# Kernel optimization log

Measured on AMD Instinct MI355X. Metric: run time of the kernel, lower is better.

The kernel has to match this reference:

```python
import jax, jax.numpy as jnp
import numpy as np
import math

LOG2 = math.log(2.0)

def shifted_softplus(x):
    return jax.nn.softplus(x) - LOG2

def setup_inputs() -> dict:
    key = jax.random.key(0)
    ks = jax.random.split(key, 12)
    n_atoms, n_pairs = 40000, 640000
    d_basis, d_filt, n_rbf = 128, 128, 20
    x = jax.random.normal(ks[0], (n_atoms, d_basis), dtype=jnp.float32)
    f_ij = jax.random.uniform(ks[1], (n_pairs, n_rbf), dtype=jnp.float32)
    idx_i = jax.random.randint(ks[2], (n_pairs,), 0, n_atoms)
    idx_j = jax.random.randint(ks[3], (n_pairs,), 0, n_atoms)
    rcut_ij = jax.random.uniform(ks[4], (n_pairs,), dtype=jnp.float32)
    s_in = 1.0 / math.sqrt(d_basis)
    s_f = 1.0 / math.sqrt(n_rbf)
    s_out = 1.0 / math.sqrt(d_filt)
    W_in = jax.random.uniform(ks[5], (d_filt, d_basis), minval=-s_in, maxval=s_in)
    b_in = jax.random.uniform(ks[6], (d_filt,), minval=-s_in, maxval=s_in)
    W_f = jax.random.uniform(ks[7], (d_filt, n_rbf), minval=-s_f, maxval=s_f)
    b_f = jax.random.uniform(ks[8], (d_filt,), minval=-s_f, maxval=s_f)
    W_out = jax.random.uniform(ks[9], (d_basis, d_filt), minval=-s_out, maxval=s_out)
    b_out = jax.random.uniform(ks[10], (d_basis,), minval=-s_out, maxval=s_out)
    return {"x": x, "f_ij": f_ij, "idx_i": idx_i, "idx_j": idx_j, "rcut_ij": rcut_ij,
            "W_in": W_in, "b_in": b_in, "W_f": W_f, "b_f": b_f, "W_out": W_out, "b_out": b_out}

def reference(x, f_ij, idx_i, idx_j, rcut_ij, W_in, b_in, W_f, b_f, W_out, b_out):
    n_atoms = x.shape[0]
    # input_to_feature: Linear(d_basis -> d_filt)
    h = x @ W_in.T + b_in                                  # [n_atoms, d_filt]
    # filter_network: Linear(n_rbf -> d_filt) + ShiftedSoftplus, scaled by cutoff
    Wij = shifted_softplus(f_ij @ W_f.T + b_f) * rcut_ij[:, None]  # [n_pairs, d_filt]
    # gather neighbor features, modulate, scatter-add back to atoms
    x_ij = h[idx_j] * Wij                                  # [n_pairs, d_filt]
    agg = jax.ops.segment_sum(x_ij, idx_i, num_segments=n_atoms)   # [n_atoms, d_filt]
    # feature_to_output: Linear(d_filt -> d_basis) + ShiftedSoftplus
    return shifted_softplus(agg @ W_out.T + b_out)
```

## Files before the change

### kernel.cpp

```cpp
#include <hip/hip_runtime.h>
#include <hip/hip_bf16.h>

typedef __hip_bfloat16 bf16;
typedef __attribute__((ext_vector_type(8))) short short8;
typedef __attribute__((ext_vector_type(4))) float f32x4;

__device__ __forceinline__ float braw2f(unsigned short u) {
    return __uint_as_float(((unsigned int)u) << 16);
}
__device__ __forceinline__ unsigned short f2braw(float f) {
    bf16 b = __float2bfloat16(f);
    return *(unsigned short*)&b;
}
__device__ __forceinline__ unsigned int pack2(float lo, float hi) {
    return (unsigned int)f2braw(lo) | ((unsigned int)f2braw(hi) << 16);
}

#define LN2F 0.69314718055994531f
__device__ __forceinline__ float ssp(float x) {
    return fmaxf(x, 0.0f) + __logf(1.0f + __expf(-fabsf(x))) - LN2F;
}

template<bool ACT, bool OUT_BF16>
__global__ __launch_bounds__(256) void linear128_mfma_kernel(
    const float* __restrict__ X, const float* __restrict__ W, const float* __restrict__ Bias,
    void* __restrict__ Yv, int n_rows)
{
    __shared__ unsigned short wls[128 * 128];
    __shared__ unsigned short xs[64 * 128];
    __shared__ float bls[128];

    const float4* W4 = (const float4*)W;
    for (int i = threadIdx.x; i < 128 * 32; i += 256) {
        float4 w = W4[i];
        ushort4 s; s.x = f2braw(w.x); s.y = f2braw(w.y); s.z = f2braw(w.z); s.w = f2braw(w.w);
        *(ushort4*)&wls[i * 4] = s;
    }
    if (threadIdx.x < 128) bls[threadIdx.x] = Bias[threadIdx.x];

    const int base = blockIdx.x * 64;
    const float4* X4 = (const float4*)X;
    for (int i = threadIdx.x; i < 64 * 32; i += 256) {
        int r = i >> 5, k4 = i & 31;
        int row = base + r;
        float4 v = (row < n_rows) ? X4[(size_t)row * 32 + k4] : make_float4(0.f, 0.f, 0.f, 0.f);
        ushort4 s; s.x = f2braw(v.x); s.y = f2braw(v.y); s.z = f2braw(v.z); s.w = f2braw(v.w);
        *(ushort4*)&xs[r * 128 + k4 * 4] = s;
    }
    __syncthreads();

    const int wv = threadIdx.x >> 6;
    const int l  = threadIdx.x & 63;
    const int lm = l & 15;
    const int lq = l >> 4;

    short8 a[4];
    #pragma unroll
    for (int kk = 0; kk < 4; ++kk)
        a[kk] = *(const short8*)&xs[(wv * 16 + lm) * 128 + kk * 32 + lq * 8];

    f32x4 acc[8];
    #pragma unroll
    for (int ct = 0; ct < 8; ++ct) {
        f32x4 c = {0.f, 0.f, 0.f, 0.f};
        #pragma unroll
        for (int kk = 0; kk < 4; ++kk) {
            short8 b = *(const short8*)&wls[(ct * 16 + lm) * 128 + kk * 32 + lq * 8];
            c = __builtin_amdgcn_mfma_f32_16x16x32_bf16(a[kk], b, c, 0, 0, 0);
        }
        acc[ct] = c;
    }

    #pragma unroll
    for (int ct = 0; ct < 8; ++ct) {
        int col = ct * 16 + lm;
        float bia = bls[col];
        #pragma unroll
        for (int r = 0; r < 4; ++r) {
            int row = base + wv * 16 + lq * 4 + r;
            if (row < n_rows) {
                float o = acc[ct][r] + bia;
                if (ACT) o = ssp(o);
                if (OUT_BF16) ((unsigned short*)Yv)[(size_t)row * 128 + col] = f2braw(o);
                else          ((float*)Yv)[(size_t)row * 128 + col] = o;
            }
        }
    }
}


__global__ __launch_bounds__(256) void zero_int_kernel(int* __restrict__ p, int n) {
    int i = blockIdx.x * 256 + threadIdx.x;
    if (i < n) p[i] = 0;
}

__global__ __launch_bounds__(256) void hist_kernel(
    const int* __restrict__ idx_i, int* __restrict__ cnt, int n_pairs, int n_atoms)
{
    for (int p = blockIdx.x * 256 + threadIdx.x; p < n_pairs; p += gridDim.x * 256) {
        int ai = idx_i[p];
        if ((unsigned)ai < (unsigned)n_atoms) atomicAdd(&cnt[ai], 1);
    }
}

__global__ __launch_bounds__(1024) void scan1_kernel(
    const int* __restrict__ cnt, int* __restrict__ offs, int* __restrict__ partials, int n)
{
    __shared__ int sm[1024];
    int t = threadIdx.x, idx = blockIdx.x * 1024 + t;
    int v = (idx < n) ? cnt[idx] : 0;
    sm[t] = v;
    __syncthreads();
    #pragma unroll
    for (int d = 1; d < 1024; d <<= 1) {
        int tmp = (t >= d) ? sm[t - d] : 0;
        __syncthreads();
        sm[t] += tmp;
        __syncthreads();
    }
    if (idx < n) offs[idx] = sm[t] - v;
    if (t == 1023) partials[blockIdx.x] = sm[1023];
}

__global__ __launch_bounds__(64) void scan2_kernel(
    int* __restrict__ partials, int* __restrict__ offs, int nb, int n)
{
    __shared__ int sm[64];
    int t = threadIdx.x;
    int v = (t < nb) ? partials[t] : 0;
    sm[t] = v;
    __syncthreads();
    #pragma unroll
    for (int d = 1; d < 64; d <<= 1) {
        int tmp = (t >= d) ? sm[t - d] : 0;
        __syncthreads();
        sm[t] += tmp;
        __syncthreads();
    }
    if (t < nb) partials[t] = sm[t] - v;
    if (t == 63) offs[n] = sm[63];
}

__global__ __launch_bounds__(1024) void scan3_kernel(
    int* __restrict__ offs, int* __restrict__ cur, const int* __restrict__ partials, int n)
{
    int idx = blockIdx.x * 1024 + threadIdx.x;
    if (idx < n) {
        int o = offs[idx] + partials[blockIdx.x];
        offs[idx] = o;
        cur[idx] = o;
    }
}

__global__ __launch_bounds__(256) void scatter_pay_kernel(
    const float* __restrict__ f_ij, const int* __restrict__ idx_i, const int* __restrict__ idx_j,
    const float* __restrict__ rcut, int* __restrict__ cur, uint4* __restrict__ pay,
    int n_pairs, int n_atoms)
{
    for (int p = blockIdx.x * 256 + threadIdx.x; p < n_pairs; p += gridDim.x * 256) {
        int ai = idx_i[p];
        if ((unsigned)ai >= (unsigned)n_atoms) continue;
        int pos = atomicAdd(&cur[ai], 1);
        const float4* fr = (const float4*)(f_ij + (size_t)p * 20);
        float4 f0 = fr[0], f1 = fr[1], f2 = fr[2], f3 = fr[3], f4 = fr[4];
        uint4 q0, q1, q2;
        q0.x = pack2(f0.x, f0.y); q0.y = pack2(f0.z, f0.w);
        q0.z = pack2(f1.x, f1.y); q0.w = pack2(f1.z, f1.w);
        q1.x = pack2(f2.x, f2.y); q1.y = pack2(f2.z, f2.w);
        q1.z = pack2(f3.x, f3.y); q1.w = pack2(f3.z, f3.w);
        q2.x = pack2(f4.x, f4.y); q2.y = pack2(f4.z, f4.w);
        q2.z = (unsigned int)idx_j[p];
        q2.w = __float_as_uint(rcut[p]);
        uint4* dst = pay + (size_t)pos * 3;
        dst[0] = q0; dst[1] = q1; dst[2] = q2;
    }
}

__global__ __launch_bounds__(256) void segment_pay_kernel(
    const uint4* __restrict__ pay, const float* __restrict__ W_f,
    const float* __restrict__ b_f, const unsigned int* __restrict__ hb32,
    const int* __restrict__ offs, float* __restrict__ agg, int n_atoms)
{
    const int wave = (blockIdx.x * 256 + threadIdx.x) >> 6;
    const int lane = threadIdx.x & 63;
    if (wave >= n_atoms) return;

    const int c0 = 2 * lane;
    float w0[20], w1[20];
    #pragma unroll
    for (int r = 0; r < 20; ++r) {
        w0[r] = W_f[c0 * 20 + r];
        w1[r] = W_f[(c0 + 1) * 20 + r];
    }
    const float b0 = b_f[c0], b1 = b_f[c0 + 1];

    const int cs = offs[wave], ce = offs[wave + 1];
    float acc0 = 0.f, acc1 = 0.f;

    int s = cs;
    for (; s + 2 <= ce; s += 2) {
        const uint4* pA = pay + (size_t)s * 3;
        const uint4* pB = pA + 3;
        uint4 qA0 = pA[0], qA1 = pA[1], qA2 = pA[2];
        uint4 qB0 = pB[0], qB1 = pB[1], qB2 = pB[2];
        unsigned int uA[10] = {qA0.x,qA0.y,qA0.z,qA0.w,qA1.x,qA1.y,qA1.z,qA1.w,qA2.x,qA2.y};
        unsigned int uB[10] = {qB0.x,qB0.y,qB0.z,qB0.w,qB1.x,qB1.y,qB1.z,qB1.w,qB2.x,qB2.y};
        float a0A = b0, a1A = b1, a0B = b0, a1B = b1;
        #pragma unroll
        for (int r = 0; r < 10; ++r) {
            float loA = __uint_as_float(uA[r] << 16);
            float hiA = __uint_as_float(uA[r] & 0xffff0000u);
            float loB = __uint_as_float(uB[r] << 16);
            float hiB = __uint_as_float(uB[r] & 0xffff0000u);
            a0A += loA * w0[2*r];     a1A += loA * w1[2*r];
            a0A += hiA * w0[2*r + 1]; a1A += hiA * w1[2*r + 1];
            a0B += loB * w0[2*r];     a1B += loB * w1[2*r];
            a0B += hiB * w0[2*r + 1]; a1B += hiB * w1[2*r + 1];
        }
        float rcA = __uint_as_float(qA2.w), rcB = __uint_as_float(qB2.w);
        float wv0A = ssp(a0A) * rcA, wv1A = ssp(a1A) * rcA;
        float wv0B = ssp(a0B) * rcB, wv1B = ssp(a1B) * rcB;
        unsigned int hA = hb32[(size_t)(int)qA2.z * 64 + lane];
        unsigned int hB = hb32[(size_t)(int)qB2.z * 64 + lane];
        acc0 += __uint_as_float(hA << 16) * wv0A + __uint_as_float(hB << 16) * wv0B;
        acc1 += __uint_as_float(hA & 0xffff0000u) * wv1A + __uint_as_float(hB & 0xffff0000u) * wv1B;
    }
    if (s < ce) {
        const uint4* pA = pay + (size_t)s * 3;
        uint4 q0 = pA[0], q1 = pA[1], q2 = pA[2];
        unsigned int u[10] = {q0.x,q0.y,q0.z,q0.w,q1.x,q1.y,q1.z,q1.w,q2.x,q2.y};
        float a0 = b0, a1 = b1;
        #pragma unroll
        for (int r = 0; r < 10; ++r) {
            float lo = __uint_as_float(u[r] << 16);
            float hi = __uint_as_float(u[r] & 0xffff0000u);
            a0 += lo * w0[2*r];     a1 += lo * w1[2*r];
            a0 += hi * w0[2*r + 1]; a1 += hi * w1[2*r + 1];
        }
        float rc = __uint_as_float(q2.w);
        float wv0 = ssp(a0) * rc, wv1 = ssp(a1) * rc;
        unsigned int h = hb32[(size_t)(int)q2.z * 64 + lane];
        acc0 += __uint_as_float(h << 16) * wv0;
        acc1 += __uint_as_float(h & 0xffff0000u) * wv1;
    }

    *(float2*)&agg[(size_t)wave * 128 + c0] = make_float2(acc0, acc1);
}

__global__ __launch_bounds__(256) void scatter_kernel(
    const int* __restrict__ idx_i, int* __restrict__ cur, int* __restrict__ perm,
    int n_pairs, int n_atoms)
{
    for (int p = blockIdx.x * 256 + threadIdx.x; p < n_pairs; p += gridDim.x * 256) {
        int ai = idx_i[p];
        if ((unsigned)ai < (unsigned)n_atoms) {
            int pos = atomicAdd(&cur[ai], 1);
            perm[pos] = p;
        }
    }
}

__global__ __launch_bounds__(256) void segment_kernel(
    const float* __restrict__ f_ij, const int* __restrict__ idx_j,
    const float* __restrict__ rcut, const float* __restrict__ W_f,
    const float* __restrict__ b_f, const unsigned short* __restrict__ hb,
    const int* __restrict__ offs, const int* __restrict__ perm,
    float* __restrict__ agg, int n_atoms)
{
    const int wave = (blockIdx.x * 256 + threadIdx.x) >> 6;
    const int lane = threadIdx.x & 63;
    if (wave >= n_atoms) return;

    float w0[20], w1[20];
    #pragma unroll
    for (int r = 0; r < 20; ++r) {
        w0[r] = W_f[lane * 20 + r];
        w1[r] = W_f[(lane + 64) * 20 + r];
    }
    const float b0 = b_f[lane], b1 = b_f[lane + 64];

    const int cs = offs[wave], ce = offs[wave + 1];
    float acc0 = 0.f, acc1 = 0.f;

    int s = cs;
    for (; s + 2 <= ce; s += 2) {
        int pA = perm[s], pB = perm[s + 1];
        int ajA = idx_j[pA], ajB = idx_j[pB];
        float rcA = rcut[pA], rcB = rcut[pB];
        const float4* frA = (const float4*)(f_ij + (size_t)pA * 20);
        const float4* frB = (const float4*)(f_ij + (size_t)pB * 20);
        float a0A = b0, a1A = b1, a0B = b0, a1B = b1;
        #pragma unroll
        for (int q = 0; q < 5; ++q) {
            float4 fA = frA[q], fB = frB[q];
            a0A += fA.x * w0[4*q+0]; a1A += fA.x * w1[4*q+0];
            a0A += fA.y * w0[4*q+1]; a1A += fA.y * w1[4*q+1];
            a0A += fA.z * w0[4*q+2]; a1A += fA.z * w1[4*q+2];
            a0A += fA.w * w0[4*q+3]; a1A += fA.w * w1[4*q+3];
            a0B += fB.x * w0[4*q+0]; a1B += fB.x * w1[4*q+0];
            a0B += fB.y * w0[4*q+1]; a1B += fB.y * w1[4*q+1];
            a0B += fB.z * w0[4*q+2]; a1B += fB.z * w1[4*q+2];
            a0B += fB.w * w0[4*q+3]; a1B += fB.w * w1[4*q+3];
        }
        float wv0A = ssp(a0A) * rcA, wv1A = ssp(a1A) * rcA;
        float wv0B = ssp(a0B) * rcB, wv1B = ssp(a1B) * rcB;
        float h0A = braw2f(hb[(size_t)ajA * 128 + lane]);
        float h1A = braw2f(hb[(size_t)ajA * 128 + 64 + lane]);
        float h0B = braw2f(hb[(size_t)ajB * 128 + lane]);
        float h1B = braw2f(hb[(size_t)ajB * 128 + 64 + lane]);
        acc0 += h0A * wv0A + h0B * wv0B;
        acc1 += h1A * wv1A + h1B * wv1B;
    }
    if (s < ce) {
        int p = perm[s];
        int aj = idx_j[p];
        float rc = rcut[p];
        const float4* fr = (const float4*)(f_ij + (size_t)p * 20);
        float a0 = b0, a1 = b1;
        #pragma unroll
        for (int q = 0; q < 5; ++q) {
            float4 fv = fr[q];
            a0 += fv.x * w0[4*q+0]; a1 += fv.x * w1[4*q+0];
            a0 += fv.y * w0[4*q+1]; a1 += fv.y * w1[4*q+1];
            a0 += fv.z * w0[4*q+2]; a1 += fv.z * w1[4*q+2];
            a0 += fv.w * w0[4*q+3]; a1 += fv.w * w1[4*q+3];
        }
        float wv0 = ssp(a0) * rc, wv1 = ssp(a1) * rc;
        acc0 += braw2f(hb[(size_t)aj * 128 + lane]) * wv0;
        acc1 += braw2f(hb[(size_t)aj * 128 + 64 + lane]) * wv1;
    }

    agg[(size_t)wave * 128 + lane]      = acc0;
    agg[(size_t)wave * 128 + 64 + lane] = acc1;
}

static inline size_t align_up(size_t v, size_t a) { return (v + a - 1) & ~(a - 1); }

extern "C" void kernel_launch(void* const* d_in, const int* in_sizes, int n_in,
                              void* d_out, int out_size, void* d_ws, size_t ws_size,
                              hipStream_t stream) {
    const float* x     = (const float*)d_in[0];
    const float* f_ij  = (const float*)d_in[1];
    const int*   idx_i = (const int*)d_in[2];
    const int*   idx_j = (const int*)d_in[3];
    const float* rcut  = (const float*)d_in[4];
    const float* W_in  = (const float*)d_in[5];
    const float* b_in  = (const float*)d_in[6];
    const float* W_f   = (const float*)d_in[7];
    const float* b_f   = (const float*)d_in[8];
    const float* W_out = (const float*)d_in[9];
    const float* b_out = (const float*)d_in[10];

    const int n_atoms = in_sizes[0] / 128;
    const int n_pairs = in_sizes[2];
    const int nscan = (n_atoms + 1023) / 1024;
    const int mfma_grid = (n_atoms + 63) / 64;

    size_t off_hb   = 0;
    size_t off_offs = align_up(off_hb + (size_t)n_atoms * 128 * 2, 16);
    size_t off_cur  = align_up(off_offs + (size_t)(n_atoms + 1) * 4, 16);
    size_t off_part = align_up(off_cur + (size_t)n_atoms * 4, 16);
    size_t off_pay  = align_up(off_part + (size_t)nscan * 4, 64);
    size_t need_pay = off_pay + (size_t)n_pairs * 48;

    if (ws_size >= need_pay) {
        unsigned short* hb = (unsigned short*)((char*)d_ws + off_hb);
        int*  offs = (int*)((char*)d_ws + off_offs);
        int*  cur  = (int*)((char*)d_ws + off_cur);
        int*  part = (int*)((char*)d_ws + off_part);
        uint4* pay = (uint4*)((char*)d_ws + off_pay);
        float* agg = (float*)d_out;

        linear128_mfma_kernel<false, true><<<dim3(mfma_grid), dim3(256), 0, stream>>>(
            x, W_in, b_in, (void*)hb, n_atoms);

        zero_int_kernel<<<dim3((n_atoms + 255) / 256), dim3(256), 0, stream>>>(cur, n_atoms);
        hist_kernel<<<dim3(1024), dim3(256), 0, stream>>>(idx_i, cur, n_pairs, n_atoms);
        scan1_kernel<<<dim3(nscan), dim3(1024), 0, stream>>>(cur, offs, part, n_atoms);
        scan2_kernel<<<dim3(1), dim3(64), 0, stream>>>(part, offs, nscan, n_atoms);
        scan3_kernel<<<dim3(nscan), dim3(1024), 0, stream>>>(offs, cur, part, n_atoms);
        scatter_pay_kernel<<<dim3(1024), dim3(256), 0, stream>>>(
            f_ij, idx_i, idx_j, rcut, cur, pay, n_pairs, n_atoms);

        segment_pay_kernel<<<dim3((n_atoms + 3) / 4), dim3(256), 0, stream>>>(
            pay, W_f, b_f, (const unsigned int*)hb, offs, agg, n_atoms);

        linear128_mfma_kernel<true, false><<<dim3(mfma_grid), dim3(256), 0, stream>>>(
            agg, W_out, b_out, d_out, n_atoms);
    } else {
        size_t o_h    = 0;
        size_t o_offs = o_h + (size_t)n_atoms * 128 * 2;
        size_t o_cur  = o_offs + (size_t)(n_atoms + 1) * 4;
        size_t o_perm = o_cur + (size_t)n_atoms * 4;
        size_t o_part = o_perm + (size_t)n_pairs * 4;
        unsigned short* hb = (unsigned short*)((char*)d_ws + o_h);
        int* offs = (int*)((char*)d_ws + o_offs);
        int* cur  = (int*)((char*)d_ws + o_cur);
        int* perm = (int*)((char*)d_ws + o_perm);
        int* part = (int*)((char*)d_ws + o_part);
        float* agg = (float*)d_out;

        linear128_mfma_kernel<false, true><<<dim3(mfma_grid), dim3(256), 0, stream>>>(
            x, W_in, b_in, (void*)hb, n_atoms);

        zero_int_kernel<<<dim3((n_atoms + 255) / 256), dim3(256), 0, stream>>>(cur, n_atoms);
        hist_kernel<<<dim3(1024), dim3(256), 0, stream>>>(idx_i, cur, n_pairs, n_atoms);
        scan1_kernel<<<dim3(nscan), dim3(1024), 0, stream>>>(cur, offs, part, n_atoms);
        scan2_kernel<<<dim3(1), dim3(64), 0, stream>>>(part, offs, nscan, n_atoms);
        scan3_kernel<<<dim3(nscan), dim3(1024), 0, stream>>>(offs, cur, part, n_atoms);
        scatter_kernel<<<dim3(1024), dim3(256), 0, stream>>>(idx_i, cur, perm, n_pairs, n_atoms);

        segment_kernel<<<dim3((n_atoms + 3) / 4), dim3(256), 0, stream>>>(
            f_ij, idx_j, rcut, W_f, b_f, hb, offs, perm, agg, n_atoms);

        linear128_mfma_kernel<true, false><<<dim3(mfma_grid), dim3(256), 0, stream>>>(
            agg, W_out, b_out, d_out, n_atoms);
    }
}
```

Measured before the change: 367.8 us.

## Compute filter weights with MFMA GEMM into fp16 buffer, then segment-reduce

Moves the per-pair filter network (20->128 linear plus shifted softplus and cutoff scaling) out of the per-atom segment kernel into a separate bf16 MFMA GEMM kernel. That kernel writes Wij as fp16 into a workspace buffer, processed in chunks sized to the available workspace. A new segment kernel then only gathers h[idx_j], multiplies by the stored Wij and accumulates across chunks. This replaces redundant scalar FMA work with matrix cores, at the cost of writing and re-reading a 128-wide fp16 tensor per pair (about 164 MB at full size) and some extra precision loss.

```diff
diff --git a/kernel.cpp b/kernel.cpp
--- a/kernel.cpp
+++ b/kernel.cpp
@@ -1,5 +1,6 @@
 #include <hip/hip_runtime.h>
 #include <hip/hip_bf16.h>
+#include <hip/hip_fp16.h>
 
 typedef __hip_bfloat16 bf16;
 typedef __attribute__((ext_vector_type(8))) short short8;
@@ -14,6 +15,10 @@
 }
 __device__ __forceinline__ unsigned int pack2(float lo, float hi) {
     return (unsigned int)f2braw(lo) | ((unsigned int)f2braw(hi) << 16);
+}
+__device__ __forceinline__ float h2f(unsigned short u) {
+    __half h = *(__half*)&u;
+    return __half2float(h);
 }
 
 #define LN2F 0.69314718055994531f
@@ -157,6 +162,9 @@
     const float* __restrict__ rcut, int* __restrict__ cur, uint4* __restrict__ pay,
     int n_pairs, int n_atoms)
 {
+    if (blockIdx.x == 0 && threadIdx.x < 204) {
+        ((int*)(pay + (size_t)n_pairs * 3))[threadIdx.x] = 0;
+    }
     for (int p = blockIdx.x * 256 + threadIdx.x; p < n_pairs; p += gridDim.x * 256) {
         int ai = idx_i[p];
         if ((unsigned)ai >= (unsigned)n_atoms) continue;
@@ -176,6 +184,110 @@
     }
 }
 
+__global__ __launch_bounds__(256) void wij_gemm_kernel(
+    const uint4* __restrict__ pay, const float* __restrict__ W_f,
+    const float* __restrict__ b_f, unsigned short* __restrict__ wij,
+    int c0, int c1)
+{
+    __shared__ unsigned short wls[128 * 40];
+    __shared__ float bls[128];
+
+    for (int i = threadIdx.x; i < 128 * 32; i += 256) {
+        int col = i >> 5, k = i & 31;
+        float v = (k < 20) ? W_f[col * 20 + k] : 0.f;
+        wls[col * 40 + k] = f2braw(v);
+    }
+    if (threadIdx.x < 128) bls[threadIdx.x] = b_f[threadIdx.x];
+    __syncthreads();
+
+    const int wv = threadIdx.x >> 6;
+    const int l  = threadIdx.x & 63;
+    const int lm = l & 15;
+    const int lq = l >> 4;
+
+    const int tile = blockIdx.x * 4 + wv;
+    const int p0 = c0 + tile * 16;
+    if (p0 >= c1) return;
+
+    const char* rec = (const char*)pay + (size_t)(p0 + lm) * 48;
+    short8 a = *(const short8*)(rec + lq * 16);
+    if (lq == 2) { a[4] = 0; a[5] = 0; a[6] = 0; a[7] = 0; }
+    if (lq == 3) { a[0]=0; a[1]=0; a[2]=0; a[3]=0; a[4]=0; a[5]=0; a[6]=0; a[7]=0; }
+
+    f32x4 acc[8];
+    #pragma unroll
+    for (int ct = 0; ct < 8; ++ct) {
+        short8 b = *(const short8*)&wls[(ct * 16 + lm) * 40 + lq * 8];
+        f32x4 z = {0.f, 0.f, 0.f, 0.f};
+        acc[ct] = __builtin_amdgcn_mfma_f32_16x16x32_bf16(a, b, z, 0, 0, 0);
+    }
+
+    float rc[4]; int pr[4];
+    #pragma unroll
+    for (int r = 0; r < 4; ++r) {
+        int p = p0 + lq * 4 + r;
+        pr[r] = p;
+        rc[r] = (p < c1) ? ((const float*)pay)[(size_t)p * 12 + 11] : 0.f;
+    }
+    #pragma unroll
+    for (int ct = 0; ct < 8; ++ct) {
+        float bia = bls[ct * 16 + lm];
+        #pragma unroll
+        for (int r = 0; r < 4; ++r) {
+            if (pr[r] < c1) {
+                float o = ssp(acc[ct][r] + bia) * rc[r];
+                __half hh = __float2half(o);
+                wij[(size_t)(pr[r] - c0) * 128 + ct * 16 + lm] = *(unsigned short*)&hh;
+            }
+        }
+    }
+}
+
+__global__ __launch_bounds__(256) void segment_mod_kernel(
+    const uint4* __restrict__ pay, const unsigned short* __restrict__ wij,
+    const unsigned int* __restrict__ hb32, const int* __restrict__ offs,
+    float* __restrict__ agg, int n_atoms, int c0, int c1, int first)
+{
+    const int wave = (blockIdx.x * 256 + threadIdx.x) >> 6;
+    const int lane = threadIdx.x & 63;
+    if (wave >= n_atoms) return;
+
+    int cs = offs[wave], ce = offs[wave + 1];
+    if (cs < c0) cs = c0;
+    if (ce > c1) ce = c1;
+
+    float acc0 = 0.f, acc1 = 0.f;
+    if (!first) {
+        if (cs >= ce) return;
+        float2 prev = *(const float2*)&agg[(size_t)wave * 128 + 2 * lane];
+        acc0 = prev.x; acc1 = prev.y;
+    }
+
+    const unsigned int* payu = (const unsigned int*)pay;
+    int s = cs;
+    for (; s + 2 <= ce; s += 2) {
+        int ajA = (int)payu[(size_t)s * 12 + 10];
+        int ajB = (int)payu[(size_t)(s + 1) * 12 + 10];
+        unsigned int wA = *(const unsigned int*)&wij[(size_t)(s - c0) * 128 + 2 * lane];
+        unsigned int wB = *(const unsigned int*)&wij[(size_t)(s + 1 - c0) * 128 + 2 * lane];
+        unsigned int hA = hb32[(size_t)ajA * 64 + lane];
+        unsigned int hB = hb32[(size_t)ajB * 64 + lane];
+        acc0 += __uint_as_float(hA << 16) * h2f((unsigned short)(wA & 0xffffu));
+        acc1 += __uint_as_float(hA & 0xffff0000u) * h2f((unsigned short)(wA >> 16));
+        acc0 += __uint_as_float(hB << 16) * h2f((unsigned short)(wB & 0xffffu));
+        acc1 += __uint_as_float(hB & 0xffff0000u) * h2f((unsigned short)(wB >> 16));
+    }
+    if (s < ce) {
+        int aj = (int)payu[(size_t)s * 12 + 10];
+        unsigned int w = *(const unsigned int*)&wij[(size_t)(s - c0) * 128 + 2 * lane];
+        unsigned int h = hb32[(size_t)aj * 64 + lane];
+        acc0 += __uint_as_float(h << 16) * h2f((unsigned short)(w & 0xffffu));
+        acc1 += __uint_as_float(h & 0xffff0000u) * h2f((unsigned short)(w >> 16));
+    }
+
+    *(float2*)&agg[(size_t)wave * 128 + 2 * lane] = make_float2(acc0, acc1);
+}
+
 __global__ __launch_bounds__(256) void segment_pay_kernel(
     const uint4* __restrict__ pay, const float* __restrict__ W_f,
     const float* __restrict__ b_f, const unsigned int* __restrict__ hb32,
@@ -362,8 +474,51 @@
     size_t off_part = align_up(off_cur + (size_t)n_atoms * 4, 16);
     size_t off_pay  = align_up(off_part + (size_t)nscan * 4, 64);
     size_t need_pay = off_pay + (size_t)n_pairs * 48;
-
-    if (ws_size >= need_pay) {
+    size_t off_wij  = align_up(off_pay + (size_t)n_pairs * 48 + 816, 256);
+
+    int max_chunk = 0;
+    if (ws_size > off_wij) {
+        size_t cap = (ws_size - off_wij) / 256;
+        if (cap > (size_t)n_pairs) cap = (size_t)n_pairs;
+        max_chunk = ((int)cap) & ~15;
+    }
+    int min_chunk = (n_pairs < 65536) ? ((n_pairs + 15) & ~15) : 65536;
+
+    if (max_chunk >= min_chunk && max_chunk > 0) {
+        unsigned short* hb  = (unsigned short*)((char*)d_ws + off_hb);
+        int*   offs = (int*)((char*)d_ws + off_offs);
+        int*   cur  = (int*)((char*)d_ws + off_cur);
+        int*   part = (int*)((char*)d_ws + off_part);
+        uint4* pay  = (uint4*)((char*)d_ws + off_pay);
+        unsigned short* wijp = (unsigned short*)((char*)d_ws + off_wij);
+        float* agg = (float*)d_out;
+
+        linear128_mfma_kernel<false, true><<<dim3(mfma_grid), dim3(256), 0, stream>>>(
+            x, W_in, b_in, (void*)hb, n_atoms);
+
+        zero_int_kernel<<<dim3((n_atoms + 255) / 256), dim3(256), 0, stream>>>(cur, n_atoms);
+        hist_kernel<<<dim3(1024), dim3(256), 0, stream>>>(idx_i, cur, n_pairs, n_atoms);
+        scan1_kernel<<<dim3(nscan), dim3(1024), 0, stream>>>(cur, offs, part, n_atoms);
+        scan2_kernel<<<dim3(1), dim3(64), 0, stream>>>(part, offs, nscan, n_atoms);
+        scan3_kernel<<<dim3(nscan), dim3(1024), 0, stream>>>(offs, cur, part, n_atoms);
+        scatter_pay_kernel<<<dim3(1024), dim3(256), 0, stream>>>(
+            f_ij, idx_i, idx_j, rcut, cur, pay, n_pairs, n_atoms);
+
+        int nchunks = (n_pairs + max_chunk - 1) / max_chunk;
+        for (int c = 0; c < nchunks; ++c) {
+            int cc0 = c * max_chunk;
+            int cc1 = cc0 + max_chunk;
+            if (cc1 > n_pairs) cc1 = n_pairs;
+            int tiles = (cc1 - cc0 + 15) / 16;
+            wij_gemm_kernel<<<dim3((tiles + 3) / 4), dim3(256), 0, stream>>>(
+                pay, W_f, b_f, wijp, cc0, cc1);
+            segment_mod_kernel<<<dim3((n_atoms + 3) / 4), dim3(256), 0, stream>>>(
+                pay, wijp, (const unsigned int*)hb, offs, agg, n_atoms, cc0, cc1, c == 0 ? 1 : 0);
+        }
+
+        linear128_mfma_kernel<true, false><<<dim3(mfma_grid), dim3(256), 0, stream>>>(
+            agg, W_out, b_out, d_out, n_atoms);
+    } else if (ws_size >= need_pay) {
         unsigned short* hb = (unsigned short*)((char*)d_ws + off_hb);
         int*  offs = (int*)((char*)d_ws + off_offs);
         int*  cur  = (int*)((char*)d_ws + off_cur);
```

After: 363.5 us. Within noise of the previous version (-1.2%).

## Fuse filter network via MFMA into pair-parallel kernel with atomic segment flush

Applied to the files above, without the earlier changes.

Adds a pair-parallel fused kernel that computes the filter network for 64 sorted pairs per block with bf16 MFMA, stores fp16 filter values in LDS, then multiplies each by the gathered neighbor features and accumulates runs of equal destination atoms, flushing with atomicAdd. This replaces the per-atom wave loop that evaluated the 20-wide filter with scalar FMAs. It needs an extra pair_atom array, a zeroing pass over the output, and atomics at segment boundaries. It also introduces fp16 rounding of the filter values.

```diff
diff --git a/kernel.cpp b/kernel.cpp
--- a/kernel.cpp
+++ b/kernel.cpp
@@ -1,5 +1,6 @@
 #include <hip/hip_runtime.h>
 #include <hip/hip_bf16.h>
+#include <hip/hip_fp16.h>
 
 typedef __hip_bfloat16 bf16;
 typedef __attribute__((ext_vector_type(8))) short short8;
@@ -14,6 +15,10 @@
 }
 __device__ __forceinline__ unsigned int pack2(float lo, float hi) {
     return (unsigned int)f2braw(lo) | ((unsigned int)f2braw(hi) << 16);
+}
+__device__ __forceinline__ float h2f(unsigned short u) {
+    __half h = *(__half*)&u;
+    return __half2float(h);
 }
 
 #define LN2F 0.69314718055994531f
@@ -152,11 +157,15 @@
     }
 }
 
+template<bool WRITE_ATOM>
 __global__ __launch_bounds__(256) void scatter_pay_kernel(
     const float* __restrict__ f_ij, const int* __restrict__ idx_i, const int* __restrict__ idx_j,
     const float* __restrict__ rcut, int* __restrict__ cur, uint4* __restrict__ pay,
-    int n_pairs, int n_atoms)
-{
+    int* __restrict__ pair_atom, int n_pairs, int n_atoms)
+{
+    if (blockIdx.x == 0 && threadIdx.x < 204) {
+        ((int*)(pay + (size_t)n_pairs * 3))[threadIdx.x] = 0;
+    }
     for (int p = blockIdx.x * 256 + threadIdx.x; p < n_pairs; p += gridDim.x * 256) {
         int ai = idx_i[p];
         if ((unsigned)ai >= (unsigned)n_atoms) continue;
@@ -173,6 +182,97 @@
         q2.w = __float_as_uint(rcut[p]);
         uint4* dst = pay + (size_t)pos * 3;
         dst[0] = q0; dst[1] = q1; dst[2] = q2;
+        if (WRITE_ATOM) pair_atom[pos] = ai;
+    }
+}
+
+__global__ __launch_bounds__(256) void fused_pair_kernel(
+    const uint4* __restrict__ pay, const int* __restrict__ pair_atom,
+    const float* __restrict__ W_f, const float* __restrict__ b_f,
+    const unsigned int* __restrict__ hb32, float* __restrict__ agg, int n_pairs)
+{
+    __shared__ unsigned short wls[128 * 40];
+    __shared__ float bls[128];
+    __shared__ unsigned short wij[64 * 132];
+    __shared__ int lds_atom[64];
+    __shared__ int lds_aj[64];
+
+    for (int i = threadIdx.x; i < 128 * 32; i += 256) {
+        int col = i >> 5, k = i & 31;
+        float v = (k < 20) ? W_f[col * 20 + k] : 0.f;
+        wls[col * 40 + k] = f2braw(v);
+    }
+    if (threadIdx.x < 128) bls[threadIdx.x] = b_f[threadIdx.x];
+
+    const int P0 = blockIdx.x * 64;
+    if (threadIdx.x < 64) {
+        int p = P0 + threadIdx.x;
+        bool valid = p < n_pairs;
+        lds_atom[threadIdx.x] = valid ? pair_atom[p] : -1;
+        lds_aj[threadIdx.x]   = valid ? (int)((const unsigned int*)pay)[(size_t)p * 12 + 10] : 0;
+    }
+    __syncthreads();
+
+    const int wv = threadIdx.x >> 6;
+    const int l  = threadIdx.x & 63;
+    const int lm = l & 15;
+    const int lq = l >> 4;
+    const int p0 = P0 + wv * 16;
+
+    if (p0 < n_pairs) {
+        const char* rec = (const char*)pay + (size_t)(p0 + lm) * 48;
+        short8 a = *(const short8*)(rec + lq * 16);
+        if (lq == 2) { a[4] = 0; a[5] = 0; a[6] = 0; a[7] = 0; }
+        if (lq == 3) { a[0]=0; a[1]=0; a[2]=0; a[3]=0; a[4]=0; a[5]=0; a[6]=0; a[7]=0; }
+
+        f32x4 acc[8];
+        #pragma unroll
+        for (int ct = 0; ct < 8; ++ct) {
+            short8 b = *(const short8*)&wls[(ct * 16 + lm) * 40 + lq * 8];
+            f32x4 z = {0.f, 0.f, 0.f, 0.f};
+            acc[ct] = __builtin_amdgcn_mfma_f32_16x16x32_bf16(a, b, z, 0, 0, 0);
+        }
+
+        float rc[4];
+        #pragma unroll
+        for (int r = 0; r < 4; ++r) {
+            int p = p0 + lq * 4 + r;
+            rc[r] = (p < n_pairs) ? ((const float*)pay)[(size_t)p * 12 + 11] : 0.f;
+        }
+        #pragma unroll
+        for (int ct = 0; ct < 8; ++ct) {
+            float bia = bls[ct * 16 + lm];
+            #pragma unroll
+            for (int r = 0; r < 4; ++r) {
+                float o = ssp(acc[ct][r] + bia) * rc[r];
+                __half hh = __float2half(o);
+                wij[(wv * 16 + lq * 4 + r) * 132 + ct * 16 + lm] = *(unsigned short*)&hh;
+            }
+        }
+    }
+    __syncthreads();
+
+    int nv = n_pairs - p0;
+    if (nv > 16) nv = 16;
+    if (nv > 0) {
+        float a0 = 0.f, a1 = 0.f;
+        int cura = lds_atom[wv * 16];
+        #pragma unroll 4
+        for (int k = 0; k < nv; ++k) {
+            int pa = lds_atom[wv * 16 + k];
+            if (pa != cura) {
+                atomicAdd(&agg[(size_t)cura * 128 + 2 * l], a0);
+                atomicAdd(&agg[(size_t)cura * 128 + 2 * l + 1], a1);
+                a0 = 0.f; a1 = 0.f; cura = pa;
+            }
+            int aj = lds_aj[wv * 16 + k];
+            unsigned int h = hb32[(size_t)aj * 64 + l];
+            unsigned int w = *(const unsigned int*)&wij[(wv * 16 + k) * 132 + 2 * l];
+            a0 += __uint_as_float(h << 16) * h2f((unsigned short)(w & 0xffffu));
+            a1 += __uint_as_float(h & 0xffff0000u) * h2f((unsigned short)(w >> 16));
+        }
+        atomicAdd(&agg[(size_t)cura * 128 + 2 * l], a0);
+        atomicAdd(&agg[(size_t)cura * 128 + 2 * l + 1], a1);
     }
 }
 
@@ -362,8 +462,38 @@
     size_t off_part = align_up(off_cur + (size_t)n_atoms * 4, 16);
     size_t off_pay  = align_up(off_part + (size_t)nscan * 4, 64);
     size_t need_pay = off_pay + (size_t)n_pairs * 48;
-
-    if (ws_size >= need_pay) {
+    size_t off_pa   = align_up(off_pay + (size_t)n_pairs * 48 + 816, 256);
+    size_t need_fused = off_pa + (size_t)(n_pairs + 64) * 4;
+
+    if (ws_size >= need_fused) {
+        unsigned short* hb  = (unsigned short*)((char*)d_ws + off_hb);
+        int*   offs = (int*)((char*)d_ws + off_offs);
+        int*   cur  = (int*)((char*)d_ws + off_cur);
+        int*   part = (int*)((char*)d_ws + off_part);
+        uint4* pay  = (uint4*)((char*)d_ws + off_pay);
+        int*   pair_atom = (int*)((char*)d_ws + off_pa);
+        float* agg = (float*)d_out;
+
+        linear128_mfma_kernel<false, true><<<dim3(mfma_grid), dim3(256), 0, stream>>>(
+            x, W_in, b_in, (void*)hb, n_atoms);
+
+        zero_int_kernel<<<dim3((n_atoms * 128 + 255) / 256), dim3(256), 0, stream>>>(
+            (int*)agg, n_atoms * 128);
+
+        zero_int_kernel<<<dim3((n_atoms + 255) / 256), dim3(256), 0, stream>>>(cur, n_atoms);
+        hist_kernel<<<dim3(1024), dim3(256), 0, stream>>>(idx_i, cur, n_pairs, n_atoms);
+        scan1_kernel<<<dim3(nscan), dim3(1024), 0, stream>>>(cur, offs, part, n_atoms);
+        scan2_kernel<<<dim3(1), dim3(64), 0, stream>>>(part, offs, nscan, n_atoms);
+        scan3_kernel<<<dim3(nscan), dim3(1024), 0, stream>>>(offs, cur, part, n_atoms);
+        scatter_pay_kernel<true><<<dim3(1024), dim3(256), 0, stream>>>(
+            f_ij, idx_i, idx_j, rcut, cur, pay, pair_atom, n_pairs, n_atoms);
+
+        fused_pair_kernel<<<dim3((n_pairs + 63) / 64), dim3(256), 0, stream>>>(
+            pay, pair_atom, W_f, b_f, (const unsigned int*)hb, agg, n_pairs);
+
+        linear128_mfma_kernel<true, false><<<dim3(mfma_grid), dim3(256), 0, stream>>>(
+            agg, W_out, b_out, d_out, n_atoms);
+    } else if (ws_size >= need_pay) {
         unsigned short* hb = (unsigned short*)((char*)d_ws + off_hb);
         int*  offs = (int*)((char*)d_ws + off_offs);
         int*  cur  = (int*)((char*)d_ws + off_cur);
@@ -379,8 +509,8 @@
         scan1_kernel<<<dim3(nscan), dim3(1024), 0, stream>>>(cur, offs, part, n_atoms);
         scan2_kernel<<<dim3(1), dim3(64), 0, stream>>>(part, offs, nscan, n_atoms);
         scan3_kernel<<<dim3(nscan), dim3(1024), 0, stream>>>(offs, cur, part, n_atoms);
-        scatter_pay_kernel<<<dim3(1024), dim3(256), 0, stream>>>(
-            f_ij, idx_i, idx_j, rcut, cur, pay, n_pairs, n_atoms);
+        scatter_pay_kernel<false><<<dim3(1024), dim3(256), 0, stream>>>(
+            f_ij, idx_i, idx_j, rcut, cur, pay, (int*)nullptr, n_pairs, n_atoms);
 
         segment_pay_kernel<<<dim3((n_atoms + 3) / 4), dim3(256), 0, stream>>>(
             pay, W_f, b_f, (const unsigned int*)hb, offs, agg, n_atoms);
```

After: 377.4 us. 2.6% more time.

## Read f_ij directly via permutation instead of packing a bf16 payload

Applied to the files above, without the earlier changes.

The scatter stage no longer copies f_ij rows into a bf16 48-byte payload per pair. It now writes only a permutation index plus (idx_j, rcut) metadata. The segment kernel gathers the fp32 f_ij row (80 bytes) through the permutation and uses fp32 filter inputs. The aim is to avoid the payload write and re-read traffic, at the cost of random 80-byte gathers and one extra indirection in the hot loop. It also loads W_f as float4 and moves the segment bounds to scalar registers with readfirstlane.

```diff
diff --git a/kernel.cpp b/kernel.cpp
--- a/kernel.cpp
+++ b/kernel.cpp
@@ -1,5 +1,6 @@
 #include <hip/hip_runtime.h>
 #include <hip/hip_bf16.h>
+#include <hip/hip_fp16.h>
 
 typedef __hip_bfloat16 bf16;
 typedef __attribute__((ext_vector_type(8))) short short8;
@@ -11,9 +12,6 @@
 __device__ __forceinline__ unsigned short f2braw(float f) {
     bf16 b = __float2bfloat16(f);
     return *(unsigned short*)&b;
-}
-__device__ __forceinline__ unsigned int pack2(float lo, float hi) {
-    return (unsigned int)f2braw(lo) | ((unsigned int)f2braw(hi) << 16);
 }
 
 #define LN2F 0.69314718055994531f
@@ -152,32 +150,25 @@
     }
 }
 
-__global__ __launch_bounds__(256) void scatter_pay_kernel(
-    const float* __restrict__ f_ij, const int* __restrict__ idx_i, const int* __restrict__ idx_j,
-    const float* __restrict__ rcut, int* __restrict__ cur, uint4* __restrict__ pay,
+__global__ __launch_bounds__(256) void scatter_meta_kernel(
+    const int* __restrict__ idx_i, const int* __restrict__ idx_j,
+    const float* __restrict__ rcut, int* __restrict__ cur,
+    int* __restrict__ perm, uint2* __restrict__ meta,
     int n_pairs, int n_atoms)
 {
     for (int p = blockIdx.x * 256 + threadIdx.x; p < n_pairs; p += gridDim.x * 256) {
         int ai = idx_i[p];
-        if ((unsigned)ai >= (unsigned)n_atoms) continue;
-        int pos = atomicAdd(&cur[ai], 1);
-        const float4* fr = (const float4*)(f_ij + (size_t)p * 20);
-        float4 f0 = fr[0], f1 = fr[1], f2 = fr[2], f3 = fr[3], f4 = fr[4];
-        uint4 q0, q1, q2;
-        q0.x = pack2(f0.x, f0.y); q0.y = pack2(f0.z, f0.w);
-        q0.z = pack2(f1.x, f1.y); q0.w = pack2(f1.z, f1.w);
-        q1.x = pack2(f2.x, f2.y); q1.y = pack2(f2.z, f2.w);
-        q1.z = pack2(f3.x, f3.y); q1.w = pack2(f3.z, f3.w);
-        q2.x = pack2(f4.x, f4.y); q2.y = pack2(f4.z, f4.w);
-        q2.z = (unsigned int)idx_j[p];
-        q2.w = __float_as_uint(rcut[p]);
-        uint4* dst = pay + (size_t)pos * 3;
-        dst[0] = q0; dst[1] = q1; dst[2] = q2;
-    }
-}
-
-__global__ __launch_bounds__(256) void segment_pay_kernel(
-    const uint4* __restrict__ pay, const float* __restrict__ W_f,
+        if ((unsigned)ai < (unsigned)n_atoms) {
+            int pos = atomicAdd(&cur[ai], 1);
+            perm[pos] = p;
+            meta[pos] = make_uint2((unsigned int)idx_j[p], __float_as_uint(rcut[p]));
+        }
+    }
+}
+
+__global__ __launch_bounds__(256) void segment_direct_kernel(
+    const float* __restrict__ f_ij, const uint2* __restrict__ meta,
+    const int* __restrict__ perm, const float* __restrict__ W_f,
     const float* __restrict__ b_f, const unsigned int* __restrict__ hb32,
     const int* __restrict__ offs, float* __restrict__ agg, int n_atoms)
 {
@@ -186,60 +177,70 @@
     if (wave >= n_atoms) return;
 
     const int c0 = 2 * lane;
-    float w0[20], w1[20];
-    #pragma unroll
-    for (int r = 0; r < 20; ++r) {
-        w0[r] = W_f[c0 * 20 + r];
-        w1[r] = W_f[(c0 + 1) * 20 + r];
+    float wt[40];
+    {
+        const float4* wf4 = (const float4*)(W_f + (size_t)c0 * 20);
+        #pragma unroll
+        for (int r = 0; r < 10; ++r) {
+            float4 v = wf4[r];
+            wt[4 * r + 0] = v.x; wt[4 * r + 1] = v.y;
+            wt[4 * r + 2] = v.z; wt[4 * r + 3] = v.w;
+        }
     }
     const float b0 = b_f[c0], b1 = b_f[c0 + 1];
 
-    const int cs = offs[wave], ce = offs[wave + 1];
+    const int cs = __builtin_amdgcn_readfirstlane(offs[wave]);
+    const int ce = __builtin_amdgcn_readfirstlane(offs[wave + 1]);
     float acc0 = 0.f, acc1 = 0.f;
 
     int s = cs;
     for (; s + 2 <= ce; s += 2) {
-        const uint4* pA = pay + (size_t)s * 3;
-        const uint4* pB = pA + 3;
-        uint4 qA0 = pA[0], qA1 = pA[1], qA2 = pA[2];
-        uint4 qB0 = pB[0], qB1 = pB[1], qB2 = pB[2];
-        unsigned int uA[10] = {qA0.x,qA0.y,qA0.z,qA0.w,qA1.x,qA1.y,qA1.z,qA1.w,qA2.x,qA2.y};
-        unsigned int uB[10] = {qB0.x,qB0.y,qB0.z,qB0.w,qB1.x,qB1.y,qB1.z,qB1.w,qB2.x,qB2.y};
+        int pA = perm[s], pB = perm[s + 1];
+        uint2 mA = meta[s], mB = meta[s + 1];
+        const uint4* frA = (const uint4*)(f_ij + (size_t)pA * 20);
+        const uint4* frB = (const uint4*)(f_ij + (size_t)pB * 20);
+        uint4 qA0 = frA[0], qA1 = frA[1], qA2 = frA[2], qA3 = frA[3], qA4 = frA[4];
+        uint4 qB0 = frB[0], qB1 = frB[1], qB2 = frB[2], qB3 = frB[3], qB4 = frB[4];
+        unsigned int uA[20] = {qA0.x,qA0.y,qA0.z,qA0.w, qA1.x,qA1.y,qA1.z,qA1.w,
+                               qA2.x,qA2.y,qA2.z,qA2.w, qA3.x,qA3.y,qA3.z,qA3.w,
+                               qA4.x,qA4.y,qA4.z,qA4.w};
+        unsigned int uB[20] = {qB0.x,qB0.y,qB0.z,qB0.w, qB1.x,qB1.y,qB1.z,qB1.w,
+                               qB2.x,qB2.y,qB2.z,qB2.w, qB3.x,qB3.y,qB3.z,qB3.w,
+                               qB4.x,qB4.y,qB4.z,qB4.w};
         float a0A = b0, a1A = b1, a0B = b0, a1B = b1;
         #pragma unroll
-        for (int r = 0; r < 10; ++r) {
-            float loA = __uint_as_float(uA[r] << 16);
-            float hiA = __uint_as_float(uA[r] & 0xffff0000u);
-            float loB = __uint_as_float(uB[r] << 16);
-            float hiB = __uint_as_float(uB[r] & 0xffff0000u);
-            a0A += loA * w0[2*r];     a1A += loA * w1[2*r];
-            a0A += hiA * w0[2*r + 1]; a1A += hiA * w1[2*r + 1];
-            a0B += loB * w0[2*r];     a1B += loB * w1[2*r];
-            a0B += hiB * w0[2*r + 1]; a1B += hiB * w1[2*r + 1];
-        }
-        float rcA = __uint_as_float(qA2.w), rcB = __uint_as_float(qB2.w);
+        for (int r = 0; r < 20; ++r) {
+            float fA = __uint_as_float(uA[r]);
+            float fB = __uint_as_float(uB[r]);
+            a0A += fA * wt[r];      a1A += fA * wt[20 + r];
+            a0B += fB * wt[r];      a1B += fB * wt[20 + r];
+        }
+        float rcA = __uint_as_float(mA.y), rcB = __uint_as_float(mB.y);
         float wv0A = ssp(a0A) * rcA, wv1A = ssp(a1A) * rcA;
         float wv0B = ssp(a0B) * rcB, wv1B = ssp(a1B) * rcB;
-        unsigned int hA = hb32[(size_t)(int)qA2.z * 64 + lane];
-        unsigned int hB = hb32[(size_t)(int)qB2.z * 64 + lane];
+        unsigned int hA = hb32[(size_t)(int)mA.x * 64 + lane];
+        unsigned int hB = hb32[(size_t)(int)mB.x * 64 + lane];
         acc0 += __uint_as_float(hA << 16) * wv0A + __uint_as_float(hB << 16) * wv0B;
         acc1 += __uint_as_float(hA & 0xffff0000u) * wv1A + __uint_as_float(hB & 0xffff0000u) * wv1B;
     }
     if (s < ce) {
-        const uint4* pA = pay + (size_t)s * 3;
-        uint4 q0 = pA[0], q1 = pA[1], q2 = pA[2];
-        unsigned int u[10] = {q0.x,q0.y,q0.z,q0.w,q1.x,q1.y,q1.z,q1.w,q2.x,q2.y};
+        int p = perm[s];
+        uint2 m = meta[s];
+        const uint4* fr = (const uint4*)(f_ij + (size_t)p * 20);
+        uint4 q0 = fr[0], q1 = fr[1], q2 = fr[2], q3 = fr[3], q4 = fr[4];
+        unsigned int u[20] = {q0.x,q0.y,q0.z,q0.w, q1.x,q1.y,q1.z,q1.w,
+                              q2.x,q2.y,q2.z,q2.w, q3.x,q3.y,q3.z,q3.w,
+                              q4.x,q4.y,q4.z,q4.w};
         float a0 = b0, a1 = b1;
         #pragma unroll
-        for (int r = 0; r < 10; ++r) {
-            float lo = __uint_as_float(u[r] << 16);
-            float hi = __uint_as_float(u[r] & 0xffff0000u);
-            a0 += lo * w0[2*r];     a1 += lo * w1[2*r];
-            a0 += hi * w0[2*r + 1]; a1 += hi * w1[2*r + 1];
-        }
-        float rc = __uint_as_float(q2.w);
+        for (int r = 0; r < 20; ++r) {
+            float f = __uint_as_float(u[r]);
+            a0 += f * wt[r];
+            a1 += f * wt[20 + r];
+        }
+        float rc = __uint_as_float(m.y);
         float wv0 = ssp(a0) * rc, wv1 = ssp(a1) * rc;
-        unsigned int h = hb32[(size_t)(int)q2.z * 64 + lane];
+        unsigned int h = hb32[(size_t)(int)m.x * 64 + lane];
         acc0 += __uint_as_float(h << 16) * wv0;
         acc1 += __uint_as_float(h & 0xffff0000u) * wv1;
     }
@@ -360,15 +361,17 @@
     size_t off_offs = align_up(off_hb + (size_t)n_atoms * 128 * 2, 16);
     size_t off_cur  = align_up(off_offs + (size_t)(n_atoms + 1) * 4, 16);
     size_t off_part = align_up(off_cur + (size_t)n_atoms * 4, 16);
-    size_t off_pay  = align_up(off_part + (size_t)nscan * 4, 64);
-    size_t need_pay = off_pay + (size_t)n_pairs * 48;
-
-    if (ws_size >= need_pay) {
+    size_t off_perm = align_up(off_part + (size_t)nscan * 4, 64);
+    size_t off_meta = align_up(off_perm + (size_t)n_pairs * 4, 64);
+    size_t need_t1  = off_meta + (size_t)n_pairs * 8;
+
+    if (ws_size >= need_t1) {
         unsigned short* hb = (unsigned short*)((char*)d_ws + off_hb);
         int*  offs = (int*)((char*)d_ws + off_offs);
         int*  cur  = (int*)((char*)d_ws + off_cur);
         int*  part = (int*)((char*)d_ws + off_part);
-        uint4* pay = (uint4*)((char*)d_ws + off_pay);
+        int*  perm = (int*)((char*)d_ws + off_perm);
+        uint2* meta = (uint2*)((char*)d_ws + off_meta);
         float* agg = (float*)d_out;
 
         linear128_mfma_kernel<false, true><<<dim3(mfma_grid), dim3(256), 0, stream>>>(
@@ -379,11 +382,11 @@
         scan1_kernel<<<dim3(nscan), dim3(1024), 0, stream>>>(cur, offs, part, n_atoms);
         scan2_kernel<<<dim3(1), dim3(64), 0, stream>>>(part, offs, nscan, n_atoms);
         scan3_kernel<<<dim3(nscan), dim3(1024), 0, stream>>>(offs, cur, part, n_atoms);
-        scatter_pay_kernel<<<dim3(1024), dim3(256), 0, stream>>>(
-            f_ij, idx_i, idx_j, rcut, cur, pay, n_pairs, n_atoms);
-
-        segment_pay_kernel<<<dim3((n_atoms + 3) / 4), dim3(256), 0, stream>>>(
-            pay, W_f, b_f, (const unsigned int*)hb, offs, agg, n_atoms);
+        scatter_meta_kernel<<<dim3(1024), dim3(256), 0, stream>>>(
+            idx_i, idx_j, rcut, cur, perm, meta, n_pairs, n_atoms);
+
+        segment_direct_kernel<<<dim3((n_atoms + 3) / 4), dim3(256), 0, stream>>>(
+            f_ij, meta, perm, W_f, b_f, (const unsigned int*)hb, offs, agg, n_atoms);
 
         linear128_mfma_kernel<true, false><<<dim3(mfma_grid), dim3(256), 0, stream>>>(
             agg, W_out, b_out, d_out, n_atoms);
```

Measured after the change: 348.7 us. -5.2%, faster.
